# Performance work log

Hardware: AMD Instinct MI355X
Metric: run time of the kernel (lower is better)

## Reference

```python
import jax, jax.numpy as jnp
import numpy as np

B, S, D, H, F, V, T, L = 64, 1024, 256, 256, 128, 50000, 64, 8
H2 = 2 * H
DIN = H2 + D + 3 * F  # 1152


def setup_inputs() -> dict:
    key = jax.random.key(0)
    ks = jax.random.split(key, 12)
    sd = 0.05
    return {
        "word_ids": jax.random.randint(ks[0], (B, S), 1, V, dtype=jnp.int32),
        "embed": jax.random.normal(ks[1], (V, D), jnp.float32) * sd,
        "encoder_outputs": jax.random.normal(ks[2], (B, S, H2), jnp.float32) * sd,
        "wconv1": jax.random.normal(ks[3], (F, 1, D), jnp.float32) * sd,
        "bconv1": jax.random.normal(ks[4], (F,), jnp.float32) * sd,
        "wconv2": jax.random.normal(ks[5], (F, 2, D), jnp.float32) * sd,
        "bconv2": jax.random.normal(ks[6], (F,), jnp.float32) * sd,
        "wconv3": jax.random.normal(ks[7], (F, 3, D), jnp.float32) * sd,
        "bconv3": jax.random.normal(ks[8], (F,), jnp.float32) * sd,
        "W_ih": jax.random.normal(ks[9], (4 * H2, DIN), jnp.float32) * sd,
        "W_hh": jax.random.normal(ks[10], (4 * H2, H2), jnp.float32) * sd,
        "W_fc": jax.random.normal(ks[11], (T, H2), jnp.float32) * sd,
        "seg_len": L,
    }


def reference(word_ids, embed, encoder_outputs, wconv1, bconv1, wconv2, bconv2,
              wconv3, bconv3, W_ih, W_hh, W_fc, seg_len):
    b, s = word_ids.shape
    d = embed.shape[1]
    h2 = encoder_outputs.shape[-1]
    h = h2 // 2
    nseg = s // seg_len

    # word features via embedding lookup (WordFeature with single 'word' feature)
    wf = embed[word_ids]                                  # [B, S, D]
    xs = wf.reshape(b, nseg, seg_len, d)                  # [B, nseg, L, D]
    c_w = xs.mean(axis=2)                                 # [B, nseg, D]
    es = encoder_outputs.reshape(b, nseg, seg_len, h2)
    c_h = es.mean(axis=2)                                 # [B, nseg, 2H]

    # char-CNN per segment: conv2d(1->F, (fs, D)) == 1D conv over time with D in-channels
    xc = xs.reshape(b * nseg, seg_len, d).transpose(0, 2, 1)  # [N, D, L]

    def conv_pool(w, bias):
        k = w.transpose(0, 2, 1)                          # [F, D, fs]
        y = jax.lax.conv_general_dilated(xc, k, window_strides=(1,),
                                         padding="VALID",
                                         dimension_numbers=("NCH", "OIH", "NCH"))
        y = jax.nn.relu(y + bias[None, :, None])
        return y.max(axis=2)                              # max-pool over time -> [N, F]

    c_x = jnp.concatenate([conv_pool(wconv1, bconv1),
                           conv_pool(wconv2, bconv2),
                           conv_pool(wconv3, bconv3)], axis=1)
    c_x = c_x.reshape(b, nseg, -1)                        # [B, nseg, 3F]

    dec_in = jnp.concatenate([c_w, c_h, c_x], axis=-1)    # [B, nseg, DIN]

    # decoder init: fwd-last / bwd-first encoder states
    h0 = jnp.concatenate([encoder_outputs[:, -1, :h], encoder_outputs[:, 0, h:]], axis=1)
    c0 = jnp.zeros_like(h0)

    def step(carry, x):
        hh, cc = carry
        gates = x @ W_ih.T + hh @ W_hh.T                  # [B, 4*2H]
        i, fg, g, o = jnp.split(gates, 4, axis=1)
        cc = jax.nn.sigmoid(fg) * cc + jax.nn.sigmoid(i) * jnp.tanh(g)
        hh = jax.nn.sigmoid(o) * jnp.tanh(cc)
        out = jax.nn.log_softmax(hh @ W_fc.T, axis=-1)
        return (hh, cc), out

    _, outs = jax.lax.scan(step, (h0, c0), dec_in.transpose(1, 0, 2))  # [nseg, B, T]
    return outs.transpose(1, 0, 2).reshape(b * nseg, -1)  # batch-major like the torch loop
```

## Files before the change

### kernel.cpp

```cpp
#include <hip/hip_runtime.h>
#include <math.h>

#define BB   64
#define SS   1024
#define DD   256
#define H2   512
#define FF   128
#define TT   64
#define NSEG 128
#define DIN  1152
#define G4   2048
#define MROWS 8192
#define MX   65536

typedef __attribute__((ext_vector_type(8))) short bf16x8;
typedef __attribute__((ext_vector_type(4))) float f32x4;

__device__ __forceinline__ unsigned short f2b(float f){
    union { float f; unsigned u; } v; v.f = f;
    unsigned r = v.u + 0x7fffu + ((v.u >> 16) & 1u);
    return (unsigned short)(r >> 16);
}
__device__ __forceinline__ float b2f(unsigned short h){
    union { unsigned u; float f; } v; v.u = ((unsigned)h) << 16;
    return v.f;
}


__global__ void k_cvt(const float* __restrict__ src, unsigned short* __restrict__ dst, int n){
    int i = blockIdx.x * 256 + threadIdx.x;
    if (i < n) dst[i] = f2b(src[i]);
}

__global__ void k_wf(const float* __restrict__ w1, const float* __restrict__ w2,
                     const float* __restrict__ w3, unsigned short* __restrict__ Wf){
    int i = blockIdx.x * 256 + threadIdx.x;
    int col = i >> 8, d = i & 255;
    float v;
    if (col < 128)      v = w1[col * 256 + d];
    else if (col < 384) { int f = (col - 128) & 127; int tap = (col - 128) >> 7; v = w2[f * 512 + tap * 256 + d]; }
    else                { int c = col - 384; int f = c & 127; int tap = c >> 7;  v = w3[f * 768 + tap * 256 + d]; }
    Wf[i] = f2b(v);
}

__global__ void k_tr_wfc(const float* __restrict__ src, float* __restrict__ dst){
    int i = blockIdx.x * 256 + threadIdx.x;
    int v = i >> 9, k = i & 511;
    dst[k * 64 + v] = src[i];
}

__global__ void k_gather(const int* __restrict__ wid, const float* __restrict__ embed,
                         unsigned short* __restrict__ X){
    int i = blockIdx.x * 256 + threadIdx.x;
    int row = i >> 6, d4 = i & 63;
    int w = wid[row];
    float4 v = *(const float4*)(embed + (size_t)w * DD + d4 * 4);
    ushort4 o; o.x = f2b(v.x); o.y = f2b(v.y); o.z = f2b(v.z); o.w = f2b(v.w);
    *(ushort4*)(X + (size_t)row * DD + d4 * 4) = o;
}

__global__ void k_cw(const unsigned short* __restrict__ X, unsigned short* __restrict__ dec){
    int i = blockIdx.x * 256 + threadIdx.x;
    int row = i >> 8, d = i & 255;
    const unsigned short* p = X + (size_t)row * 8 * DD + d;
    float s = 0.f;
#pragma unroll
    for (int t = 0; t < 8; t++) s += b2f(p[t * DD]);
    dec[(size_t)row * DIN + d] = f2b(s * 0.125f);
}

__global__ void k_ch(const float* __restrict__ enc, unsigned short* __restrict__ dec){
    int i = blockIdx.x * 256 + threadIdx.x;
    int row = i >> 9, c = i & 511;
    const float* p = enc + (size_t)row * 8 * H2 + c;
    float s = 0.f;
#pragma unroll
    for (int t = 0; t < 8; t++) s += p[t * H2];
    dec[(size_t)row * DIN + 256 + c] = f2b(s * 0.125f);
}

__global__ void k_h0(const float* __restrict__ enc, unsigned short* __restrict__ Hbuf){
    int i = blockIdx.x * 256 + threadIdx.x;
    int b = i >> 9, c = i & 511;
    float v = (c < 256) ? enc[(size_t)b * SS * H2 + (size_t)(SS - 1) * H2 + c]
                        : enc[(size_t)b * SS * H2 + c];
    Hbuf[(size_t)(c >> 3) * 512 + b * 8 + (c & 7)] = f2b(v);
}

__global__ __launch_bounds__(256) void gemm_bt(
    const unsigned short* __restrict__ A, const unsigned short* __restrict__ Bm,
    unsigned short* __restrict__ C, int M, int N, int K)
{
    __shared__ unsigned short As[128][40];
    __shared__ unsigned short Bs[128][40];
    const int tid = threadIdx.x;
    const int m0 = blockIdx.y * 128, n0 = blockIdx.x * 128;
    const int w = tid >> 6, lane = tid & 63;
    const int lm = lane & 15, quad = lane >> 4;
    const int wm = (w >> 1) * 64, wn = (w & 1) * 64;

    const f32x4 z = {0.f, 0.f, 0.f, 0.f};
    f32x4 acc[4][4];
#pragma unroll
    for (int i = 0; i < 4; i++)
#pragma unroll
        for (int j = 0; j < 4; j++) acc[i][j] = z;

    const int r0 = tid >> 2;
    const int kp = (tid & 3) * 8;

    for (int kc = 0; kc < K; kc += 32){
        uint4 a0 = *(const uint4*)(A + (size_t)(m0 + r0) * K + kc + kp);
        uint4 a1 = *(const uint4*)(A + (size_t)(m0 + 64 + r0) * K + kc + kp);
        uint4 b0 = *(const uint4*)(Bm + (size_t)(n0 + r0) * K + kc + kp);
        uint4 b1 = *(const uint4*)(Bm + (size_t)(n0 + 64 + r0) * K + kc + kp);
        __syncthreads();
        *(uint4*)&As[r0][kp] = a0;
        *(uint4*)&As[64 + r0][kp] = a1;
        *(uint4*)&Bs[r0][kp] = b0;
        *(uint4*)&Bs[64 + r0][kp] = b1;
        __syncthreads();
        bf16x8 af[4], bf[4];
#pragma unroll
        for (int mt = 0; mt < 4; mt++) af[mt] = *(const bf16x8*)&As[wm + mt * 16 + lm][quad * 8];
#pragma unroll
        for (int nt = 0; nt < 4; nt++) bf[nt] = *(const bf16x8*)&Bs[wn + nt * 16 + lm][quad * 8];
#pragma unroll
        for (int mt = 0; mt < 4; mt++)
#pragma unroll
            for (int nt = 0; nt < 4; nt++)
                acc[mt][nt] = __builtin_amdgcn_mfma_f32_16x16x32_bf16(af[mt], bf[nt], acc[mt][nt], 0, 0, 0);
    }
#pragma unroll
    for (int mt = 0; mt < 4; mt++){
        int mrow = m0 + wm + mt * 16 + quad * 4;
#pragma unroll
        for (int nt = 0; nt < 4; nt++){
            int ncol = n0 + wn + nt * 16 + lm;
#pragma unroll
            for (int r = 0; r < 4; r++)
                C[(size_t)(mrow + r) * N + ncol] = f2b(acc[mt][nt][r]);
        }
    }
}

__global__ __launch_bounds__(256) void gemm_bt_gates(
    const unsigned short* __restrict__ A, const unsigned short* __restrict__ Bm,
    unsigned short* __restrict__ C, int M, int N, int K)
{
    __shared__ unsigned short As[128][40];
    __shared__ unsigned short Bs[128][40];
    const int tid = threadIdx.x;
    const int m0 = blockIdx.y * 128, n0 = blockIdx.x * 128;
    const int w = tid >> 6, lane = tid & 63;
    const int lm = lane & 15, quad = lane >> 4;
    const int wm = (w >> 1) * 64, wn = (w & 1) * 64;

    const f32x4 z = {0.f, 0.f, 0.f, 0.f};
    f32x4 acc[4][4];
#pragma unroll
    for (int i = 0; i < 4; i++)
#pragma unroll
        for (int j = 0; j < 4; j++) acc[i][j] = z;

    const int r0 = tid >> 2;
    const int kp = (tid & 3) * 8;

    for (int kc = 0; kc < K; kc += 32){
        uint4 a0 = *(const uint4*)(A + (size_t)(m0 + r0) * K + kc + kp);
        uint4 a1 = *(const uint4*)(A + (size_t)(m0 + 64 + r0) * K + kc + kp);
        uint4 b0 = *(const uint4*)(Bm + (size_t)(n0 + r0) * K + kc + kp);
        uint4 b1 = *(const uint4*)(Bm + (size_t)(n0 + 64 + r0) * K + kc + kp);
        __syncthreads();
        *(uint4*)&As[r0][kp] = a0;
        *(uint4*)&As[64 + r0][kp] = a1;
        *(uint4*)&Bs[r0][kp] = b0;
        *(uint4*)&Bs[64 + r0][kp] = b1;
        __syncthreads();
        bf16x8 af[4], bf[4];
#pragma unroll
        for (int mt = 0; mt < 4; mt++) af[mt] = *(const bf16x8*)&As[wm + mt * 16 + lm][quad * 8];
#pragma unroll
        for (int nt = 0; nt < 4; nt++) bf[nt] = *(const bf16x8*)&Bs[wn + nt * 16 + lm][quad * 8];
#pragma unroll
        for (int mt = 0; mt < 4; mt++)
#pragma unroll
            for (int nt = 0; nt < 4; nt++)
                acc[mt][nt] = __builtin_amdgcn_mfma_f32_16x16x32_bf16(af[mt], bf[nt], acc[mt][nt], 0, 0, 0);
    }
#pragma unroll
    for (int mt = 0; mt < 4; mt++){
        int mrow = m0 + wm + mt * 16 + quad * 4;
#pragma unroll
        for (int nt = 0; nt < 4; nt++){
            int ncol = n0 + wn + nt * 16 + lm;
            int cb = (ncol >> 3) & 63, g = ncol >> 9, j = ncol & 7;
#pragma unroll
            for (int r = 0; r < 4; r++){
                int m = mrow + r;
                int b = m >> 7, t = m & 127;
                size_t dst = ((((size_t)cb * NSEG + t) * 64 + b) * 4 + g) * 8 + j;
                C[dst] = f2b(acc[mt][nt][r]);
            }
        }
    }
}

__global__ void k_pool(const unsigned short* __restrict__ G, const float* __restrict__ bias,
                       unsigned short* __restrict__ dec, int taps, int colofs){
    int i = blockIdx.x * 256 + threadIdx.x;
    int row = i >> 7, f = i & 127;
    int N = taps * 128;
    float mx = -1e30f;
    for (int t = 0; t <= 8 - taps; t++){
        float a = 0.f;
        for (int tap = 0; tap < taps; tap++)
            a += b2f(G[(size_t)(row * 8 + t + tap) * N + tap * 128 + f]);
        mx = fmaxf(mx, a);
    }
    mx = fmaxf(mx + bias[f], 0.f);
    dec[(size_t)row * DIN + 768 + colofs + f] = f2b(mx);
}

__global__ __launch_bounds__(256, 1) void k_lstm(
    const unsigned short* __restrict__ gxt,
    const unsigned short* __restrict__ Whh,
    unsigned short* __restrict__ Hbuf,
    int* flags)
{
    __shared__ unsigned short Wl[32][520];
    const int tid = threadIdx.x;
    const int cb = blockIdx.x;
    const int c0 = cb * 8;
    const int w = tid >> 6, lane = tid & 63, lm = lane & 15, quad = lane >> 4;

#pragma unroll
    for (int i = 0; i < 8; i++){
        int u = tid + i * 256;
        int r = u >> 6, k8 = (u & 63) * 8;
        int g = r >> 3, c = r & 7;
        *(uint4*)&Wl[r][k8] = *(const uint4*)(Whh + (size_t)(g * H2 + c0 + c) * H2 + k8);
    }
    __syncthreads();

    float cst[4] = {0.f, 0.f, 0.f, 0.f};

    for (int t = 0; t < NSEG; t++){
        float pre[4][4];
        if (lm < 8){
            const unsigned short* gp = gxt + ((size_t)cb * NSEG + t) * 2048
                                           + (w * 16 + quad * 4) * 32 + lm;
#pragma unroll
            for (int r = 0; r < 4; r++)
#pragma unroll
                for (int g = 0; g < 4; g++)
                    pre[r][g] = b2f(gp[r * 32 + g * 8]);
        }

        if (t > 0){
            if (w == 0){
                int* fp = flags + (t - 1) * 64 + lane;
                while (!__hip_atomic_load(fp, __ATOMIC_RELAXED, __HIP_MEMORY_SCOPE_AGENT))
                    __builtin_amdgcn_s_sleep(1);
            }
            __syncthreads();
        }

        const unsigned short* hp = Hbuf + (size_t)t * (BB * H2);
        f32x4 acc0 = {0.f,0.f,0.f,0.f}, acc1 = {0.f,0.f,0.f,0.f};
#pragma unroll
        for (int ks = 0; ks < 16; ks++){
            const unsigned long long* ap =
                (const unsigned long long*)(hp + (size_t)(ks * 4 + quad) * 512 + (w * 16 + lm) * 8);
            union { unsigned long long q[2]; bf16x8 v; } u;
            u.q[0] = __hip_atomic_load(ap,     __ATOMIC_RELAXED, __HIP_MEMORY_SCOPE_AGENT);
            u.q[1] = __hip_atomic_load(ap + 1, __ATOMIC_RELAXED, __HIP_MEMORY_SCOPE_AGENT);
            bf16x8 av = u.v;
            bf16x8 b0 = *(const bf16x8*)&Wl[lm][ks * 32 + quad * 8];
            bf16x8 b1 = *(const bf16x8*)&Wl[16 + lm][ks * 32 + quad * 8];
            acc0 = __builtin_amdgcn_mfma_f32_16x16x32_bf16(av, b0, acc0, 0, 0, 0);
            acc1 = __builtin_amdgcn_mfma_f32_16x16x32_bf16(av, b1, acc1, 0, 0, 0);
        }
        float p0[4], p1[4];
#pragma unroll
        for (int r = 0; r < 4; r++){
            p0[r] = __shfl_xor(acc0[r], 8);
            p1[r] = __shfl_xor(acc1[r], 8);
        }
        if (lm < 8){
            unsigned short* hwbase = Hbuf + (size_t)(t + 1) * (BB * H2) + (size_t)cb * 512;
#pragma unroll
            for (int r = 0; r < 4; r++){
                int b = w * 16 + quad * 4 + r;
                float iv = acc0[r] + pre[r][0];
                float fv = p0[r]   + pre[r][1];
                float gv = acc1[r] + pre[r][2];
                float ov = p1[r]   + pre[r][3];
                float si = 1.f / (1.f + expf(-iv));
                float sf = 1.f / (1.f + expf(-fv));
                float so = 1.f / (1.f + expf(-ov));
                cst[r] = sf * cst[r] + si * tanhf(gv);
                unsigned short hv16 = f2b(so * tanhf(cst[r]));
                unsigned short prt = (unsigned short)__shfl_xor((int)hv16, 1);
                if (!(lm & 1)){
                    unsigned int packed = (unsigned)hv16 | ((unsigned)prt << 16);
                    __hip_atomic_store((unsigned int*)(hwbase + b * 8 + lm), packed,
                                       __ATOMIC_RELAXED, __HIP_MEMORY_SCOPE_AGENT);
                }
            }
        }
        __syncthreads();
        if (tid == 0)
            __hip_atomic_store(flags + t * 64 + cb, 1, __ATOMIC_RELAXED, __HIP_MEMORY_SCOPE_AGENT);
    }
}

__global__ __launch_bounds__(256) void k_out(
    const unsigned short* __restrict__ Hbuf, const float* __restrict__ Wt, float* __restrict__ out)
{
    __shared__ float hsh[4][H2];
    const int w = threadIdx.x >> 6, lane = threadIdx.x & 63;
    const int row = blockIdx.x * 4 + w;
    const int b = row >> 7, t = row & 127;
    const unsigned short* hp = Hbuf + (size_t)(t + 1) * (BB * H2) + b * 8;
    uint4 hv = *(const uint4*)(hp + (size_t)lane * 512);
    const unsigned short* hs = (const unsigned short*)&hv;
#pragma unroll
    for (int i = 0; i < 8; i++) hsh[w][lane * 8 + i] = b2f(hs[i]);
    __syncthreads();
    float acc = 0.f;
#pragma unroll 8
    for (int k = 0; k < H2; k++)
        acc = fmaf(hsh[w][k], Wt[k * 64 + lane], acc);
    float m = acc;
#pragma unroll
    for (int off = 32; off; off >>= 1) m = fmaxf(m, __shfl_xor(m, off));
    float e = expf(acc - m), s = e;
#pragma unroll
    for (int off = 32; off; off >>= 1) s += __shfl_xor(s, off);
    out[(size_t)row * TT + lane] = acc - m - logf(s);
}

extern "C" void kernel_launch(void* const* d_in, const int* in_sizes, int n_in,
                              void* d_out, int out_size, void* d_ws, size_t ws_size,
                              hipStream_t stream)
{
    const int*   wid = (const int*)d_in[0];
    const float* emb = (const float*)d_in[1];
    const float* enc = (const float*)d_in[2];
    const float* wc1 = (const float*)d_in[3];
    const float* bc1 = (const float*)d_in[4];
    const float* wc2 = (const float*)d_in[5];
    const float* bc2 = (const float*)d_in[6];
    const float* wc3 = (const float*)d_in[7];
    const float* bc3 = (const float*)d_in[8];
    const float* wih = (const float*)d_in[9];
    const float* whh = (const float*)d_in[10];
    const float* wfc = (const float*)d_in[11];

    char* ws = (char*)d_ws;
    size_t off = 0;
    auto alloc = [&](size_t bytes) -> void* {
        void* p = ws + off; off += (bytes + 255) & ~(size_t)255; return p;
    };
    unsigned short* X    = (unsigned short*)alloc((size_t)MX * DD * 2);
    unsigned short* dec  = (unsigned short*)alloc((size_t)MROWS * DIN * 2);
    unsigned short* Gb   = (unsigned short*)alloc((size_t)MX * 384 * 2);
    unsigned short* Wfb  = (unsigned short*)alloc((size_t)768 * 256 * 2);
    unsigned short* Wihb = (unsigned short*)alloc((size_t)G4 * DIN * 2);
    unsigned short* Whhb = (unsigned short*)alloc((size_t)G4 * H2 * 2);
    float*          Wfct = (float*)alloc((size_t)H2 * TT * 4);
    int*            flags = (int*)alloc((size_t)NSEG * 64 * 4);
    unsigned short* Hbuf  = X;
    unsigned short* gates = Gb;

    hipMemsetAsync(flags, 0, (size_t)NSEG * 64 * 4, stream);
    k_cvt<<<(G4 * DIN + 255) / 256, 256, 0, stream>>>(wih, Wihb, G4 * DIN);
    k_cvt<<<(G4 * H2 + 255) / 256, 256, 0, stream>>>(whh, Whhb, G4 * H2);
    k_wf<<<768, 256, 0, stream>>>(wc1, wc2, wc3, Wfb);
    k_tr_wfc<<<128, 256, 0, stream>>>(wfc, Wfct);
    k_gather<<<MX / 4, 256, 0, stream>>>(wid, emb, X);
    k_cw<<<MROWS, 256, 0, stream>>>(X, dec);
    k_ch<<<MROWS * 2, 256, 0, stream>>>(enc, dec);

    gemm_bt<<<dim3(1, 512), 256, 0, stream>>>(X, Wfb,                         Gb, MX, 128, 256);
    k_pool<<<4096, 256, 0, stream>>>(Gb, bc1, dec, 1, 0);
    gemm_bt<<<dim3(2, 512), 256, 0, stream>>>(X, Wfb + (size_t)128 * 256,     Gb, MX, 256, 256);
    k_pool<<<4096, 256, 0, stream>>>(Gb, bc2, dec, 2, 128);
    gemm_bt<<<dim3(3, 512), 256, 0, stream>>>(X, Wfb + (size_t)384 * 256,     Gb, MX, 384, 256);
    k_pool<<<4096, 256, 0, stream>>>(Gb, bc3, dec, 3, 256);

    k_h0<<<BB * H2 / 256, 256, 0, stream>>>(enc, Hbuf);
    gemm_bt_gates<<<dim3(16, 64), 256, 0, stream>>>(dec, Wihb, gates, MROWS, G4, DIN);
    k_lstm<<<64, 256, 0, stream>>>(gates, Whhb, Hbuf, flags);
    k_out<<<2048, 256, 0, stream>>>(Hbuf, Wfct, (float*)d_out);
}
```

Before: 1.036 ms.

## Replace per-step flag barrier in LSTM with sentinel-valued hidden-state polling

The persistent LSTM kernel no longer waits on per-step completion flags, a block-wide barrier and a flag store. The hidden-state buffer is now pre-filled with a 0xAAAA sentinel, and each wave polls its own h operand chunks until none holds the sentinel. Writers remap any real value equal to 0xAAAA to 0xAAAB. This removes the two __syncthreads and the flag round-trip from the serial recurrence. The costs are an extra memset of the whole history buffer, a tiny numeric perturbation, and reliance on relaxed atomics with per-half-word visibility.

```diff
diff --git a/kernel.cpp b/kernel.cpp
--- a/kernel.cpp
+++ b/kernel.cpp
@@ -25,6 +25,10 @@
     union { unsigned u; float f; } v; v.u = ((unsigned)h) << 16;
     return v.f;
 }
+__device__ __forceinline__ bool has_aa(unsigned long long x){
+    unsigned long long y = x ^ 0xAAAAAAAAAAAAAAAAULL;
+    return ((y - 0x0001000100010001ULL) & ~y & 0x8000800080008000ULL) != 0ULL;
+}
 
 
 __global__ void k_cvt(const float* __restrict__ src, unsigned short* __restrict__ dst, int n){
@@ -84,7 +88,9 @@
     int b = i >> 9, c = i & 511;
     float v = (c < 256) ? enc[(size_t)b * SS * H2 + (size_t)(SS - 1) * H2 + c]
                         : enc[(size_t)b * SS * H2 + c];
-    Hbuf[(size_t)(c >> 3) * 512 + b * 8 + (c & 7)] = f2b(v);
+    unsigned short hv = f2b(v);
+    if (hv == 0xAAAAu) hv = 0xAAABu;
+    Hbuf[(size_t)(c >> 3) * 512 + b * 8 + (c & 7)] = hv;
 }
 
 __global__ __launch_bounds__(256) void gemm_bt(
@@ -225,8 +231,7 @@
 __global__ __launch_bounds__(256, 1) void k_lstm(
     const unsigned short* __restrict__ gxt,
     const unsigned short* __restrict__ Whh,
-    unsigned short* __restrict__ Hbuf,
-    int* flags)
+    unsigned short* __restrict__ Hbuf)
 {
     __shared__ unsigned short Wl[32][520];
     const int tid = threadIdx.x;
@@ -257,24 +262,32 @@
                     pre[r][g] = b2f(gp[r * 32 + g * 8]);
         }
 
-        if (t > 0){
-            if (w == 0){
-                int* fp = flags + (t - 1) * 64 + lane;
-                while (!__hip_atomic_load(fp, __ATOMIC_RELAXED, __HIP_MEMORY_SCOPE_AGENT))
-                    __builtin_amdgcn_s_sleep(1);
-            }
-            __syncthreads();
-        }
-
-        const unsigned short* hp = Hbuf + (size_t)t * (BB * H2);
-        f32x4 acc0 = {0.f,0.f,0.f,0.f}, acc1 = {0.f,0.f,0.f,0.f};
+        const unsigned short* hp = Hbuf + (size_t)t * (BB * H2) + (w * 16 + lm) * 8;
+        unsigned long long q0[16], q1[16];
 #pragma unroll
         for (int ks = 0; ks < 16; ks++){
             const unsigned long long* ap =
-                (const unsigned long long*)(hp + (size_t)(ks * 4 + quad) * 512 + (w * 16 + lm) * 8);
+                (const unsigned long long*)(hp + (size_t)(ks * 4 + quad) * 512);
+            q0[ks] = __hip_atomic_load(ap,     __ATOMIC_RELAXED, __HIP_MEMORY_SCOPE_AGENT);
+            q1[ks] = __hip_atomic_load(ap + 1, __ATOMIC_RELAXED, __HIP_MEMORY_SCOPE_AGENT);
+        }
+#pragma unroll
+        for (int ks = 0; ks < 16; ks++){
+            if (has_aa(q0[ks]) || has_aa(q1[ks])){
+                const unsigned long long* ap =
+                    (const unsigned long long*)(hp + (size_t)(ks * 4 + quad) * 512);
+                do {
+                    q0[ks] = __hip_atomic_load(ap,     __ATOMIC_RELAXED, __HIP_MEMORY_SCOPE_AGENT);
+                    q1[ks] = __hip_atomic_load(ap + 1, __ATOMIC_RELAXED, __HIP_MEMORY_SCOPE_AGENT);
+                } while (has_aa(q0[ks]) || has_aa(q1[ks]));
+            }
+        }
+
+        f32x4 acc0 = {0.f,0.f,0.f,0.f}, acc1 = {0.f,0.f,0.f,0.f};
+#pragma unroll
+        for (int ks = 0; ks < 16; ks++){
             union { unsigned long long q[2]; bf16x8 v; } u;
-            u.q[0] = __hip_atomic_load(ap,     __ATOMIC_RELAXED, __HIP_MEMORY_SCOPE_AGENT);
-            u.q[1] = __hip_atomic_load(ap + 1, __ATOMIC_RELAXED, __HIP_MEMORY_SCOPE_AGENT);
+            u.q[0] = q0[ks]; u.q[1] = q1[ks];
             bf16x8 av = u.v;
             bf16x8 b0 = *(const bf16x8*)&Wl[lm][ks * 32 + quad * 8];
             bf16x8 b1 = *(const bf16x8*)&Wl[16 + lm][ks * 32 + quad * 8];
@@ -301,6 +314,7 @@
                 float so = 1.f / (1.f + expf(-ov));
                 cst[r] = sf * cst[r] + si * tanhf(gv);
                 unsigned short hv16 = f2b(so * tanhf(cst[r]));
+                if (hv16 == 0xAAAAu) hv16 = 0xAAABu;
                 unsigned short prt = (unsigned short)__shfl_xor((int)hv16, 1);
                 if (!(lm & 1)){
                     unsigned int packed = (unsigned)hv16 | ((unsigned)prt << 16);
@@ -309,9 +323,6 @@
                 }
             }
         }
-        __syncthreads();
-        if (tid == 0)
-            __hip_atomic_store(flags + t * 64 + cb, 1, __ATOMIC_RELAXED, __HIP_MEMORY_SCOPE_AGENT);
     }
 }
 
@@ -370,11 +381,9 @@
     unsigned short* Wihb = (unsigned short*)alloc((size_t)G4 * DIN * 2);
     unsigned short* Whhb = (unsigned short*)alloc((size_t)G4 * H2 * 2);
     float*          Wfct = (float*)alloc((size_t)H2 * TT * 4);
-    int*            flags = (int*)alloc((size_t)NSEG * 64 * 4);
     unsigned short* Hbuf  = X;
     unsigned short* gates = Gb;
 
-    hipMemsetAsync(flags, 0, (size_t)NSEG * 64 * 4, stream);
     k_cvt<<<(G4 * DIN + 255) / 256, 256, 0, stream>>>(wih, Wihb, G4 * DIN);
     k_cvt<<<(G4 * H2 + 255) / 256, 256, 0, stream>>>(whh, Whhb, G4 * H2);
     k_wf<<<768, 256, 0, stream>>>(wc1, wc2, wc3, Wfb);
@@ -390,8 +399,9 @@
     gemm_bt<<<dim3(3, 512), 256, 0, stream>>>(X, Wfb + (size_t)384 * 256,     Gb, MX, 384, 256);
     k_pool<<<4096, 256, 0, stream>>>(Gb, bc3, dec, 3, 256);
 
+    hipMemsetAsync(Hbuf + (size_t)BB * H2, 0xAA, (size_t)NSEG * BB * H2 * 2, stream);
     k_h0<<<BB * H2 / 256, 256, 0, stream>>>(enc, Hbuf);
     gemm_bt_gates<<<dim3(16, 64), 256, 0, stream>>>(dec, Wihb, gates, MROWS, G4, DIN);
-    k_lstm<<<64, 256, 0, stream>>>(gates, Whhb, Hbuf, flags);
+    k_lstm<<<64, 256, 0, stream>>>(gates, Whhb, Hbuf);
     k_out<<<2048, 256, 0, stream>>>(Hbuf, Wfct, (float*)d_out);
 }
```

Result: slower. 1.550 ms (+49.6%).
